# Optimization experiments

Hardware: AMD Instinct MI355X
Metric: run time of the kernel (lower is better)

The kernel has to match this reference:

```python
import jax, jax.numpy as jnp
import numpy as np
from jax import lax

GROUP = 8
EPS = 1e-5

def _bn_relu(x, gamma, beta):
    # BatchNorm3d in train mode: batch stats over (N,D,H,W) per channel, then ReLU
    mean = x.mean(axis=(0, 2, 3, 4), keepdims=True)
    var = x.var(axis=(0, 2, 3, 4), keepdims=True)
    xn = (x - mean) * lax.rsqrt(var + EPS)
    return jax.nn.relu(xn * gamma[None, :, None, None, None] + beta[None, :, None, None, None])

def _group_norm(x, gamma, beta):
    # GroupNorm(cg, cg): one channel per group -> per (n,c) normalization over spatial dims
    mean = x.mean(axis=(2, 3, 4), keepdims=True)
    var = x.var(axis=(2, 3, 4), keepdims=True)
    xn = (x - mean) * lax.rsqrt(var + EPS)
    return xn * gamma[None, :, None, None, None] + beta[None, :, None, None, None]

def setup_inputs() -> dict:
    key = jax.random.key(0)
    ks = jax.random.split(key, 4)
    b, c, d, h, w = 2, 64, 64, 64, 64
    cg = c // GROUP
    return {
        "x": jax.random.normal(ks[0], (b, c, d, h, w), dtype=jnp.float32),
        "conv1_w": jax.random.normal(ks[1], (cg, cg, 1, 1, 1), dtype=jnp.float32) * 0.1,
        "conv1_b": jnp.zeros((cg,), jnp.float32),
        "bn1_g": jnp.ones((cg,), jnp.float32),
        "bn1_b": jnp.zeros((cg,), jnp.float32),
        "conv3_w": jax.random.normal(ks[2], (cg, cg, 3, 3, 3), dtype=jnp.float32) * 0.05,
        "conv3_b": jnp.zeros((cg,), jnp.float32),
        "bn3_g": jnp.ones((cg,), jnp.float32),
        "bn3_b": jnp.zeros((cg,), jnp.float32),
        "gn_g": jnp.ones((cg,), jnp.float32),
        "gn_b": jnp.zeros((cg,), jnp.float32),
    }

def reference(x, conv1_w, conv1_b, bn1_g, bn1_b, conv3_w, conv3_b, bn3_g, bn3_b, gn_g, gn_b):
    b, c, d, h, w = x.shape
    g = GROUP
    cg = c // g
    gx = x.reshape(b * g, cg, d, h, w)

    # directional average pools -> all stacked along axis 2 as length-(d+h+w) profiles
    x_h = gx.mean(axis=(3, 4), keepdims=True)                      # (bg,cg,d,1,1)
    x_w = gx.mean(axis=(2, 4), keepdims=True).transpose(0, 1, 3, 2, 4)  # (bg,cg,h,1,1)
    x_d = gx.mean(axis=(2, 3), keepdims=True).transpose(0, 1, 4, 3, 2)  # (bg,cg,w,1,1)
    cat = jnp.concatenate([x_h, x_w, x_d], axis=2)                 # (bg,cg,d+h+w,1,1)

    # 1x1x1 conv == channel mix, then BN+ReLU
    hwd = jnp.einsum('oi,bisuv->bosuv', conv1_w[:, :, 0, 0, 0], cat) + conv1_b[None, :, None, None, None]
    hwd = _bn_relu(hwd, bn1_g, bn1_b)

    a_h = jax.nn.sigmoid(hwd[:, :, :d]).reshape(b * g, cg, d, 1, 1)
    a_w = jax.nn.sigmoid(hwd[:, :, d:d + h]).reshape(b * g, cg, 1, h, 1)
    a_d = jax.nn.sigmoid(hwd[:, :, d + h:]).reshape(b * g, cg, 1, 1, w)

    x1 = _group_norm(gx * (a_h * a_w * a_d), gn_g, gn_b)           # (bg,cg,d,h,w)

    x2 = lax.conv_general_dilated(gx, conv3_w, (1, 1, 1), 'SAME',
                                  dimension_numbers=('NCDHW', 'OIDHW', 'NCDHW'))
    x2 = _bn_relu(x2 + conv3_b[None, :, None, None, None], bn3_g, bn3_b)

    x11 = jax.nn.softmax(x1.mean(axis=(2, 3, 4)), axis=-1)         # (bg,cg)
    x21 = jax.nn.softmax(x2.mean(axis=(2, 3, 4)), axis=-1)         # (bg,cg)
    x12 = x1.reshape(b * g, cg, d * h * w)
    x22 = x2.reshape(b * g, cg, d * h * w)

    weights = (jnp.einsum('bc,bcn->bn', x11, x22) +
               jnp.einsum('bc,bcn->bn', x21, x12)).reshape(b * g, 1, d, h, w)
    return (gx * jax.nn.sigmoid(weights)).reshape(b, c, d, h, w)
```

## Files before the change

kernel.cpp:

```cpp
#include <hip/hip_runtime.h>
#include <math.h>
#include <stdint.h>

#define VOL 262144
#define EPSF 1e-5f

typedef _Float16 half4_t __attribute__((ext_vector_type(4)));
typedef _Float16 half8 __attribute__((ext_vector_type(8)));
typedef float floatx4 __attribute__((ext_vector_type(4)));

__device__ __forceinline__ float waveReduceSum(float v) {
    #pragma unroll
    for (int off = 32; off > 0; off >>= 1) v += __shfl_down(v, off);
    return v;
}

__device__ __forceinline__ uint32_t pk2(float a, float b) {
    uint32_t r;
    asm("v_cvt_pkrtz_f16_f32 %0, %1, %2" : "=v"(r) : "v"(a), "v"(b));
    return r;
}

__global__ void k_wprep(const float* __restrict__ w3, _Float16* __restrict__ wB) {
    int i = blockIdx.x * 256 + threadIdx.x;
    if (i < 3584) {
        int j = i & 7;
        int lane = (i >> 3) & 63;
        int ks = i >> 9;
        int oc = lane & 15;
        int t = ks * 4 + (lane >> 4);
        float v = 0.f;
        if (oc < 8 && t < 27) v = w3[(oc * 8 + j) * 27 + t];
        wB[i] = (_Float16)v;
    }
}

__global__ void k_pools(const float* __restrict__ x, float* __restrict__ catS) {
    int r = blockIdx.x >> 3, part = blockIdx.x & 7;
    const float* base = x + (size_t)r * VOL + ((size_t)(part * 8) << 12);
    __shared__ float sd[8], sh[64], sw[64];
    int tid = threadIdx.x;
    if (tid < 8) sd[tid] = 0.f;
    if (tid < 64) { sh[tid] = 0.f; sw[tid] = 0.f; }
    __syncthreads();
    int w4 = (tid & 15) * 4;
    int hr = tid >> 4;
    float dacc[8];
    float hacc[4] = {0.f, 0.f, 0.f, 0.f};
    float wacc[4] = {0.f, 0.f, 0.f, 0.f};
    #pragma unroll
    for (int p = 0; p < 8; p++) dacc[p] = 0.f;
    #pragma unroll
    for (int p = 0; p < 8; p++) {
        const float* pd = base + (p << 12);
        #pragma unroll
        for (int j = 0; j < 4; j++) {
            float4 v = *(const float4*)(pd + ((hr + j * 16) << 6) + w4);
            float s = v.x + v.y + v.z + v.w;
            dacc[p] += s; hacc[j] += s;
            wacc[0] += v.x; wacc[1] += v.y; wacc[2] += v.z; wacc[3] += v.w;
        }
    }
    #pragma unroll
    for (int p = 0; p < 8; p++) {
        float s = waveReduceSum(dacc[p]);
        if ((tid & 63) == 0) atomicAdd(&sd[p], s);
    }
    #pragma unroll
    for (int j = 0; j < 4; j++) atomicAdd(&sh[hr + j * 16], hacc[j]);
    #pragma unroll
    for (int k = 0; k < 4; k++) atomicAdd(&sw[w4 + k], wacc[k]);
    __syncthreads();
    float* o = catS + (size_t)r * 192;
    if (tid < 8)                       atomicAdd(&o[part * 8 + tid], sd[tid]);
    else if (tid >= 64 && tid < 128)   atomicAdd(&o[64 + tid - 64], sh[tid - 64]);
    else if (tid >= 128 && tid < 192)  atomicAdd(&o[128 + tid - 128], sw[tid - 128]);
}

__global__ void k_attn_stats(const float* __restrict__ catS, const float* __restrict__ w1,
                             const float* __restrict__ b1, const float* __restrict__ g1,
                             const float* __restrict__ be1, float* __restrict__ attnp) {
    __shared__ float r1[256], r2[256];
    __shared__ float wsm[64];
    int tid = threadIdx.x;
    if (tid < 64) wsm[tid] = w1[tid] * (1.f / 4096.f);
    __syncthreads();
    int o = tid >> 5, j = tid & 31;
    float s1 = 0.f, s2 = 0.f;
    for (int idx = j; idx < 3072; idx += 32) {
        int bgI = idx / 192, s = idx - bgI * 192;
        const float* cp = catS + (size_t)bgI * 1536 + s;
        float h = b1[o];
        #pragma unroll
        for (int i = 0; i < 8; i++) h += wsm[o * 8 + i] * cp[i * 192];
        s1 += h; s2 += h * h;
    }
    r1[tid] = s1; r2[tid] = s2;
    __syncthreads();
    for (int st = 16; st > 0; st >>= 1) {
        if (j < st) { r1[tid] += r1[tid + st]; r2[tid] += r2[tid + st]; }
        __syncthreads();
    }
    if (j == 0) {
        float mean = r1[tid] / 3072.f;
        float var  = r2[tid] / 3072.f - mean * mean;
        float sc = g1[o] * rsqrtf(var + EPSF);
        attnp[o] = sc; attnp[8 + o] = be1[o] - mean * sc;
    }
}

__global__ void k_attn_apply(const float* __restrict__ catS, const float* __restrict__ w1,
                             const float* __restrict__ b1, const float* __restrict__ attnp,
                             float* __restrict__ aout) {
    __shared__ float wsm[64];
    int tid = threadIdx.x;
    if (tid < 64) wsm[tid] = w1[tid] * (1.f / 4096.f);
    __syncthreads();
    int e = blockIdx.x * 256 + tid;
    int bgI = e / 1536;
    int rem = e - bgI * 1536;
    int oo = rem / 192;
    int s = rem - oo * 192;
    const float* cp = catS + (size_t)bgI * 1536 + s;
    float h = b1[oo];
    #pragma unroll
    for (int i = 0; i < 8; i++) h += wsm[oo * 8 + i] * cp[i * 192];
    float v = attnp[oo] * h + attnp[8 + oo];
    v = fmaxf(v, 0.f);
    aout[e] = 1.f / (1.f + __expf(-v));
}

__global__ void k_gnstats(const float* __restrict__ x, const float* __restrict__ a,
                          float* __restrict__ gs) {
    int r = blockIdx.x >> 3, part = blockIdx.x & 7;
    const float* xp = x + (size_t)r * VOL + ((size_t)part << 15);
    __shared__ float A[192];
    __shared__ float wred[8];
    int tid = threadIdx.x;
    if (tid < 192) A[tid] = a[(size_t)r * 192 + tid];
    __syncthreads();
    float s1 = 0.f, s2 = 0.f;
    for (int it = 0; it < 32; it++) {
        int e4 = it * 256 + tid;
        int n = e4 * 4;
        int dl = n >> 12;
        int h = (n >> 6) & 63, w = n & 63;
        float4 v = *(const float4*)(xp + n);
        float adh = A[part * 8 + dl] * A[64 + h];
        float y0 = v.x * adh * A[128 + w];
        float y1 = v.y * adh * A[128 + w + 1];
        float y2 = v.z * adh * A[128 + w + 2];
        float y3 = v.w * adh * A[128 + w + 3];
        s1 += y0 + y1 + y2 + y3;
        s2 += y0 * y0 + y1 * y1 + y2 * y2 + y3 * y3;
    }
    s1 = waveReduceSum(s1); s2 = waveReduceSum(s2);
    int lane = tid & 63, wid = tid >> 6;
    if (lane == 0) { wred[wid] = s1; wred[4 + wid] = s2; }
    __syncthreads();
    if (tid == 0) {
        atomicAdd(&gs[r],       wred[0] + wred[1] + wred[2] + wred[3]);
        atomicAdd(&gs[128 + r], wred[4] + wred[5] + wred[6] + wred[7]);
    }
}

#define SLICE_B (18 * 66 * 16)

__device__ __forceinline__ void stage_slice(const float* __restrict__ xb, int dd,
                                            char* smem, int slot, int h0, int tid) {
    char* sb = smem + slot * SLICE_B;
    bool dok = (dd >= 0) && (dd < 64);
    const float* pd = xb + ((size_t)(dd & 63) << 12);
    for (int u = tid; u < 288; u += 256) {
        int hl = u >> 4;
        int w4 = (u & 15) << 2;
        int gh = h0 - 1 + hl;
        bool ok = dok && (gh >= 0) && (gh < 64);
        float vv[8][4];
        #pragma unroll
        for (int ic = 0; ic < 8; ic++) {
            float4 t = make_float4(0.f, 0.f, 0.f, 0.f);
            if (ok) t = *(const float4*)(pd + ((size_t)ic << 18) + (gh << 6) + w4);
            vv[ic][0] = t.x; vv[ic][1] = t.y; vv[ic][2] = t.z; vv[ic][3] = t.w;
        }
        char* wp = sb + ((hl * 66) + 1 + w4) * 16;
        #pragma unroll
        for (int j = 0; j < 4; j++) {
            uint4 q;
            q.x = pk2(vv[0][j], vv[1][j]);
            q.y = pk2(vv[2][j], vv[3][j]);
            q.z = pk2(vv[4][j], vv[5][j]);
            q.w = pk2(vv[6][j], vv[7][j]);
            *(uint4*)(wp + j * 16) = q;
        }
    }
}

__global__ __launch_bounds__(256) void k_conv(const float* __restrict__ x,
                                              const _Float16* __restrict__ wB,
                                              const float* __restrict__ b3,
                                              _Float16* __restrict__ x2h,
                                              float* __restrict__ stats) {
    __shared__ __align__(16) char smem[3 * SLICE_B + 512];
    float* wred = (float*)(smem + 3 * SLICE_B);
    int blk = blockIdx.x;
    int bg = blk >> 5;
    int rem = blk & 31;
    int ht = rem >> 3;
    int dc = rem & 7;
    int h0 = ht << 4;
    int d0 = dc << 3;
    int tid = threadIdx.x;
    int lane = tid & 63, wid = tid >> 6;
    int lm = lane & 15, lg = lane >> 4;
    const float* xb = x + ((size_t)bg << 21);

    half8 bfr[7];
    #pragma unroll
    for (int ks = 0; ks < 7; ks++)
        bfr[ks] = *(const half8*)(wB + (ks << 9) + (lane << 3));

    float b3v = (lm < 8) ? b3[lm] : 0.f;

    int rel[7], kzv[7];
    #pragma unroll
    for (int ks = 0; ks < 7; ks++) {
        int t = ks * 4 + lg; if (t > 26) t = 26;
        int kz = t / 9, r9 = t - kz * 9;
        int ky = r9 / 3, kx = r9 - ky * 3;
        kzv[ks] = kz;
        rel[ks] = (((ky + wid * 4) * 66) + kx + lm) << 4;
    }

    for (int u = tid; u < 108; u += 256) {
        int s = u / 36, r2 = u - s * 36;
        int hh = r2 >> 1, side = r2 & 1;
        uint4 z; z.x = 0; z.y = 0; z.z = 0; z.w = 0;
        *(uint4*)(smem + s * SLICE_B + ((hh * 66) + side * 65) * 16) = z;
    }

    size_t eb = (((size_t)(bg * 8 + lm)) << 18) + ((size_t)(h0 + wid * 4) << 6) + (lg << 2);
    bool ocok = lm < 8;
    float ps = 0.f, pq = 0.f;

    stage_slice(xb, d0 - 1, smem, (d0 + 2) % 3, h0, tid);
    stage_slice(xb, d0,     smem, d0 % 3,       h0, tid);
    __syncthreads();

    for (int i = 0; i < 8; i++) {
        int d = d0 + i;
        stage_slice(xb, d + 1, smem, (d + 1) % 3, h0, tid);
        __syncthreads();
        int u0 = ((d + 2) % 3) * SLICE_B;
        int u1 = (d % 3) * SLICE_B;
        int u2 = ((d + 1) % 3) * SLICE_B;
        int ab[7];
        #pragma unroll
        for (int ks = 0; ks < 7; ks++)
            ab[ks] = (kzv[ks] == 0 ? u0 : (kzv[ks] == 1 ? u1 : u2)) + rel[ks];
        #pragma unroll
        for (int ri = 0; ri < 4; ri++) {
            #pragma unroll
            for (int wt = 0; wt < 4; wt++) {
                floatx4 acc = {b3v, b3v, b3v, b3v};
                #pragma unroll
                for (int ks = 0; ks < 7; ks++) {
                    half8 af = *(const half8*)(smem + ab[ks] + ((ri * 66 + wt * 16) << 4));
                    acc = __builtin_amdgcn_mfma_f32_16x16x32_f16(af, bfr[ks], acc, 0, 0, 0);
                }
                uint32_t q0 = pk2(acc[0], acc[1]);
                uint32_t q1 = pk2(acc[2], acc[3]);
                if (ocok) {
                    uint2 st; st.x = q0; st.y = q1;
                    *(uint2*)(x2h + eb + ((size_t)d << 12) + (ri << 6) + (wt << 4)) = st;
                }
                ps += acc[0] + acc[1] + acc[2] + acc[3];
                pq += acc[0] * acc[0] + acc[1] * acc[1] + acc[2] * acc[2] + acc[3] * acc[3];
            }
        }
        __syncthreads();
    }

    ps += __shfl_xor(ps, 16); ps += __shfl_xor(ps, 32);
    pq += __shfl_xor(pq, 16); pq += __shfl_xor(pq, 32);
    if (lane < 16) { wred[wid * 32 + lm] = ps; wred[wid * 32 + 16 + lm] = pq; }
    __syncthreads();
    if (tid < 8) {
        float t1 = wred[tid] + wred[32 + tid] + wred[64 + tid] + wred[96 + tid];
        float t2 = wred[16 + tid] + wred[48 + tid] + wred[80 + tid] + wred[112 + tid];
        atomicAdd(&stats[tid], t1);
        atomicAdd(&stats[8 + tid], t2);
    }
}

__global__ void k_finalize(const float* __restrict__ stats, const float* __restrict__ g3,
                           const float* __restrict__ be3, const float* __restrict__ gnb,
                           float* __restrict__ bnp, float* __restrict__ x11) {
    int tid = threadIdx.x;
    if (tid < 8) {
        float N = 16.f * (float)VOL;
        float mean = stats[tid] / N;
        float var  = stats[8 + tid] / N - mean * mean;
        float sc = g3[tid] * rsqrtf(var + EPSF);
        bnp[tid] = sc; bnp[8 + tid] = be3[tid] - mean * sc;
    }
    if (tid == 0) {
        float m = -1e30f;
        for (int c = 0; c < 8; c++) m = fmaxf(m, gnb[c]);
        float e[8], sum = 0.f;
        for (int c = 0; c < 8; c++) { e[c] = __expf(gnb[c] - m); sum += e[c]; }
        for (int c = 0; c < 8; c++) x11[c] = e[c] / sum;
    }
}

__global__ void k_relumean(const _Float16* __restrict__ x2h, const float* __restrict__ bnp,
                           float* __restrict__ mrelu) {
    int blk = blockIdx.x;
    int r = blk >> 3, part = blk & 7;
    int cc = r & 7;
    float sc = bnp[cc], sh = bnp[8 + cc];
    const half4_t* p = (const half4_t*)(x2h + (size_t)r * VOL + (size_t)part * 32768);
    int tid = threadIdx.x;
    float s = 0.f;
    for (int it = 0; it < 32; it++) {
        half4_t v = p[it * 256 + tid];
        s += fmaxf(sc * (float)v.x + sh, 0.f) + fmaxf(sc * (float)v.y + sh, 0.f)
           + fmaxf(sc * (float)v.z + sh, 0.f) + fmaxf(sc * (float)v.w + sh, 0.f);
    }
    s = waveReduceSum(s);
    __shared__ float wred[4];
    int lane = tid & 63, wid = tid >> 6;
    if (lane == 0) wred[wid] = s;
    __syncthreads();
    if (tid == 0) atomicAdd(&mrelu[r], wred[0] + wred[1] + wred[2] + wred[3]);
}

__global__ void k_soft21(const float* __restrict__ mrelu, float* __restrict__ x21) {
    int bg = threadIdx.x;
    if (bg < 16) {
        float v[8], m = -1e30f;
        for (int c = 0; c < 8; c++) { v[c] = mrelu[bg * 8 + c] / (float)VOL; m = fmaxf(m, v[c]); }
        float sum = 0.f;
        for (int c = 0; c < 8; c++) { v[c] = __expf(v[c] - m); sum += v[c]; }
        for (int c = 0; c < 8; c++) x21[bg * 8 + c] = v[c] / sum;
    }
}

__global__ void k_final(const float* __restrict__ x, const _Float16* __restrict__ x2h,
                        const float* __restrict__ a, const float* __restrict__ bnp,
                        const float* __restrict__ x11g, const float* __restrict__ x21g,
                        const float* __restrict__ gs, const float* __restrict__ gng,
                        const float* __restrict__ gnb, float* __restrict__ out) {
    int bg = blockIdx.x >> 8;
    int seg = blockIdx.x & 255;
    int tid = threadIdx.x;
    __shared__ float sa[1536];
    __shared__ float sc_[8], sh_[8], sx11[8], sx21[8], sgsc[8], sgsh[8];
    const float* ap = a + (size_t)bg * 1536;
    for (int i = tid; i < 1536; i += 256) sa[i] = ap[i];
    if (tid < 8) {
        int r = bg * 8 + tid;
        sc_[tid] = bnp[tid]; sh_[tid] = bnp[8 + tid];
        sx11[tid] = x11g[tid]; sx21[tid] = x21g[r];
        float mean = gs[r] / (float)VOL;
        float var  = gs[128 + r] / (float)VOL - mean * mean;
        float gr = rsqrtf(var + EPSF) * gng[tid];
        sgsc[tid] = gr; sgsh[tid] = gnb[tid] - mean * gr;
    }
    __syncthreads();
    int n = (seg * 256 + tid) * 4;
    int d = n >> 12, h = (n >> 6) & 63, w = n & 63;
    size_t base = ((size_t)bg << 21) + n;
    float4 xr[8];
    float w0 = 0.f, w1 = 0.f, w2 = 0.f, w3 = 0.f;
    #pragma unroll
    for (int c = 0; c < 8; c++) {
        size_t idx = base + ((size_t)c << 18);
        float4 xv = *(const float4*)(x + idx);
        half4_t v2 = *(const half4_t*)(x2h + idx);
        xr[c] = xv;
        float adh = sa[c * 192 + d] * sa[c * 192 + 64 + h] * sgsc[c];
        float x22_0 = fmaxf(sc_[c] * (float)v2.x + sh_[c], 0.f);
        float x22_1 = fmaxf(sc_[c] * (float)v2.y + sh_[c], 0.f);
        float x22_2 = fmaxf(sc_[c] * (float)v2.z + sh_[c], 0.f);
        float x22_3 = fmaxf(sc_[c] * (float)v2.w + sh_[c], 0.f);
        float x12_0 = xv.x * (adh * sa[c * 192 + 128 + w])     + sgsh[c];
        float x12_1 = xv.y * (adh * sa[c * 192 + 128 + w + 1]) + sgsh[c];
        float x12_2 = xv.z * (adh * sa[c * 192 + 128 + w + 2]) + sgsh[c];
        float x12_3 = xv.w * (adh * sa[c * 192 + 128 + w + 3]) + sgsh[c];
        w0 += sx11[c] * x22_0 + sx21[c] * x12_0;
        w1 += sx11[c] * x22_1 + sx21[c] * x12_1;
        w2 += sx11[c] * x22_2 + sx21[c] * x12_2;
        w3 += sx11[c] * x22_3 + sx21[c] * x12_3;
    }
    float s0 = 1.f / (1.f + __expf(-w0));
    float s1 = 1.f / (1.f + __expf(-w1));
    float s2 = 1.f / (1.f + __expf(-w2));
    float s3 = 1.f / (1.f + __expf(-w3));
    #pragma unroll
    for (int c = 0; c < 8; c++) {
        float4 o;
        o.x = xr[c].x * s0; o.y = xr[c].y * s1; o.z = xr[c].z * s2; o.w = xr[c].w * s3;
        *(float4*)(out + base + ((size_t)c << 18)) = o;
    }
}

extern "C" void kernel_launch(void* const* d_in, const int* in_sizes, int n_in,
                              void* d_out, int out_size, void* d_ws, size_t ws_size,
                              hipStream_t stream) {
    const float* x   = (const float*)d_in[0];
    const float* w1  = (const float*)d_in[1];
    const float* b1  = (const float*)d_in[2];
    const float* g1  = (const float*)d_in[3];
    const float* be1 = (const float*)d_in[4];
    const float* w3  = (const float*)d_in[5];
    const float* b3  = (const float*)d_in[6];
    const float* g3  = (const float*)d_in[7];
    const float* be3 = (const float*)d_in[8];
    const float* gng = (const float*)d_in[9];
    const float* gnb = (const float*)d_in[10];
    float* out = (float*)d_out;

    float* wsf       = (float*)d_ws;
    _Float16* x2h    = (_Float16*)d_ws;
    float* catS   = wsf + 16777216;
    float* stats  = catS + 24576;
    float* gs     = stats + 16;
    float* mrelu  = gs + 256;
    float* a      = mrelu + 128;
    float* bnp    = a + 24576;
    float* x11    = bnp + 16;
    float* x21    = x11 + 8;
    float* attnp  = x21 + 128;
    _Float16* wB  = (_Float16*)(attnp + 16);

    hipMemsetAsync(catS, 0, (24576 + 16 + 256 + 128) * sizeof(float), stream);

    k_wprep     <<<14, 256, 0, stream>>>(w3, wB);
    k_pools     <<<1024, 256, 0, stream>>>(x, catS);
    k_attn_stats<<<1, 256, 0, stream>>>(catS, w1, b1, g1, be1, attnp);
    k_attn_apply<<<96, 256, 0, stream>>>(catS, w1, b1, attnp, a);
    k_gnstats   <<<1024, 256, 0, stream>>>(x, a, gs);
    k_conv      <<<512, 256, 0, stream>>>(x, wB, b3, x2h, stats);
    k_finalize  <<<1, 64, 0, stream>>>(stats, g3, be3, gnb, bnp, x11);
    k_relumean  <<<1024, 256, 0, stream>>>(x2h, bnp, mrelu);
    k_soft21    <<<1, 64, 0, stream>>>(mrelu, x21);
    k_final     <<<4096, 256, 0, stream>>>(x, x2h, a, bnp, x11, x21, gs, gng, gnb, out);
}
```

Before: 453.6 us.

## Fuse GroupNorm statistics into conv staging and shuffle-reduce pool partials

Removes the separate k_gnstats kernel, which re-read all of x. The conv kernel now accumulates per-channel GroupNorm sums and squared sums while staging x slices, using the attention vectors loaded into shared memory. The pools kernel doubles its grid with 4 depth slices per block and pre-reduces h and w partials with wave shuffles before the shared atomics. This saves one full pass over x in exchange for more register pressure and shared memory in the MFMA conv kernel.

```diff
diff --git a/kernel.cpp b/kernel.cpp
--- a/kernel.cpp
+++ b/kernel.cpp
@@ -36,22 +36,21 @@
 }
 
 __global__ void k_pools(const float* __restrict__ x, float* __restrict__ catS) {
-    int r = blockIdx.x >> 3, part = blockIdx.x & 7;
-    const float* base = x + (size_t)r * VOL + ((size_t)(part * 8) << 12);
-    __shared__ float sd[8], sh[64], sw[64];
-    int tid = threadIdx.x;
-    if (tid < 8) sd[tid] = 0.f;
+    int r = blockIdx.x >> 4, p4 = blockIdx.x & 15;
+    const float* base = x + (size_t)r * VOL + ((size_t)(p4 * 4) << 12);
+    __shared__ float sd[4], sh[64], sw[64];
+    int tid = threadIdx.x;
+    if (tid < 4) sd[tid] = 0.f;
     if (tid < 64) { sh[tid] = 0.f; sw[tid] = 0.f; }
     __syncthreads();
     int w4 = (tid & 15) * 4;
     int hr = tid >> 4;
-    float dacc[8];
+    int lane = tid & 63;
+    float dacc[4] = {0.f, 0.f, 0.f, 0.f};
     float hacc[4] = {0.f, 0.f, 0.f, 0.f};
     float wacc[4] = {0.f, 0.f, 0.f, 0.f};
     #pragma unroll
-    for (int p = 0; p < 8; p++) dacc[p] = 0.f;
-    #pragma unroll
-    for (int p = 0; p < 8; p++) {
+    for (int p = 0; p < 4; p++) {
         const float* pd = base + (p << 12);
         #pragma unroll
         for (int j = 0; j < 4; j++) {
@@ -62,17 +61,26 @@
         }
     }
     #pragma unroll
-    for (int p = 0; p < 8; p++) {
+    for (int p = 0; p < 4; p++) {
         float s = waveReduceSum(dacc[p]);
-        if ((tid & 63) == 0) atomicAdd(&sd[p], s);
-    }
-    #pragma unroll
-    for (int j = 0; j < 4; j++) atomicAdd(&sh[hr + j * 16], hacc[j]);
-    #pragma unroll
-    for (int k = 0; k < 4; k++) atomicAdd(&sw[w4 + k], wacc[k]);
+        if (lane == 0) atomicAdd(&sd[p], s);
+    }
+    #pragma unroll
+    for (int j = 0; j < 4; j++) {
+        float hv = hacc[j];
+        hv += __shfl_xor(hv, 1); hv += __shfl_xor(hv, 2);
+        hv += __shfl_xor(hv, 4); hv += __shfl_xor(hv, 8);
+        if ((lane & 15) == 0) atomicAdd(&sh[hr + j * 16], hv);
+    }
+    #pragma unroll
+    for (int k = 0; k < 4; k++) {
+        float wv = wacc[k];
+        wv += __shfl_xor(wv, 16); wv += __shfl_xor(wv, 32);
+        if (lane < 16) atomicAdd(&sw[w4 + k], wv);
+    }
     __syncthreads();
     float* o = catS + (size_t)r * 192;
-    if (tid < 8)                       atomicAdd(&o[part * 8 + tid], sd[tid]);
+    if (tid < 4)                       atomicAdd(&o[p4 * 4 + tid], sd[tid]);
     else if (tid >= 64 && tid < 128)   atomicAdd(&o[64 + tid - 64], sh[tid - 64]);
     else if (tid >= 128 && tid < 192)  atomicAdd(&o[128 + tid - 128], sw[tid - 128]);
 }
@@ -130,58 +138,41 @@
     aout[e] = 1.f / (1.f + __expf(-v));
 }
 
-__global__ void k_gnstats(const float* __restrict__ x, const float* __restrict__ a,
-                          float* __restrict__ gs) {
-    int r = blockIdx.x >> 3, part = blockIdx.x & 7;
-    const float* xp = x + (size_t)r * VOL + ((size_t)part << 15);
-    __shared__ float A[192];
-    __shared__ float wred[8];
-    int tid = threadIdx.x;
-    if (tid < 192) A[tid] = a[(size_t)r * 192 + tid];
-    __syncthreads();
-    float s1 = 0.f, s2 = 0.f;
-    for (int it = 0; it < 32; it++) {
-        int e4 = it * 256 + tid;
-        int n = e4 * 4;
-        int dl = n >> 12;
-        int h = (n >> 6) & 63, w = n & 63;
-        float4 v = *(const float4*)(xp + n);
-        float adh = A[part * 8 + dl] * A[64 + h];
-        float y0 = v.x * adh * A[128 + w];
-        float y1 = v.y * adh * A[128 + w + 1];
-        float y2 = v.z * adh * A[128 + w + 2];
-        float y3 = v.w * adh * A[128 + w + 3];
-        s1 += y0 + y1 + y2 + y3;
-        s2 += y0 * y0 + y1 * y1 + y2 * y2 + y3 * y3;
-    }
-    s1 = waveReduceSum(s1); s2 = waveReduceSum(s2);
-    int lane = tid & 63, wid = tid >> 6;
-    if (lane == 0) { wred[wid] = s1; wred[4 + wid] = s2; }
-    __syncthreads();
-    if (tid == 0) {
-        atomicAdd(&gs[r],       wred[0] + wred[1] + wred[2] + wred[3]);
-        atomicAdd(&gs[128 + r], wred[4] + wred[5] + wred[6] + wred[7]);
-    }
-}
-
 #define SLICE_B (18 * 66 * 16)
 
 __device__ __forceinline__ void stage_slice(const float* __restrict__ xb, int dd,
-                                            char* smem, int slot, int h0, int tid) {
+                                            char* smem, int slot, int h0, int tid,
+                                            const float* __restrict__ sA, int d0,
+                                            float* g1, float* g2) {
     char* sb = smem + slot * SLICE_B;
     bool dok = (dd >= 0) && (dd < 64);
+    bool core = (dd >= d0) && (dd < d0 + 8);
     const float* pd = xb + ((size_t)(dd & 63) << 12);
     for (int u = tid; u < 288; u += 256) {
         int hl = u >> 4;
         int w4 = (u & 15) << 2;
         int gh = h0 - 1 + hl;
         bool ok = dok && (gh >= 0) && (gh < 64);
+        bool acc = core && (hl >= 1) && (hl <= 16);
         float vv[8][4];
         #pragma unroll
         for (int ic = 0; ic < 8; ic++) {
             float4 t = make_float4(0.f, 0.f, 0.f, 0.f);
             if (ok) t = *(const float4*)(pd + ((size_t)ic << 18) + (gh << 6) + w4);
             vv[ic][0] = t.x; vv[ic][1] = t.y; vv[ic][2] = t.z; vv[ic][3] = t.w;
+        }
+        if (acc) {
+            #pragma unroll
+            for (int ic = 0; ic < 8; ic++) {
+                const float* Ap = sA + ic * 192;
+                float ad = Ap[dd] * Ap[64 + gh];
+                float y0 = vv[ic][0] * ad * Ap[128 + w4];
+                float y1 = vv[ic][1] * ad * Ap[128 + w4 + 1];
+                float y2 = vv[ic][2] * ad * Ap[128 + w4 + 2];
+                float y3 = vv[ic][3] * ad * Ap[128 + w4 + 3];
+                g1[ic] += y0 + y1 + y2 + y3;
+                g2[ic] += y0 * y0 + y1 * y1 + y2 * y2 + y3 * y3;
+            }
         }
         char* wp = sb + ((hl * 66) + 1 + w4) * 16;
         #pragma unroll
@@ -199,10 +190,14 @@
 __global__ __launch_bounds__(256) void k_conv(const float* __restrict__ x,
                                               const _Float16* __restrict__ wB,
                                               const float* __restrict__ b3,
+                                              const float* __restrict__ a,
                                               _Float16* __restrict__ x2h,
-                                              float* __restrict__ stats) {
-    __shared__ __align__(16) char smem[3 * SLICE_B + 512];
+                                              float* __restrict__ stats,
+                                              float* __restrict__ gs) {
+    __shared__ __align__(16) char smem[3 * SLICE_B + 768 + 6144];
     float* wred = (float*)(smem + 3 * SLICE_B);
+    float* wgn  = wred + 128;
+    float* sA   = (float*)(smem + 3 * SLICE_B + 768);
     int blk = blockIdx.x;
     int bg = blk >> 5;
     int rem = blk & 31;
@@ -238,18 +233,22 @@
         uint4 z; z.x = 0; z.y = 0; z.z = 0; z.w = 0;
         *(uint4*)(smem + s * SLICE_B + ((hh * 66) + side * 65) * 16) = z;
     }
+    for (int i = tid; i < 1536; i += 256) sA[i] = a[(size_t)bg * 1536 + i];
+    __syncthreads();
 
     size_t eb = (((size_t)(bg * 8 + lm)) << 18) + ((size_t)(h0 + wid * 4) << 6) + (lg << 2);
     bool ocok = lm < 8;
     float ps = 0.f, pq = 0.f;
-
-    stage_slice(xb, d0 - 1, smem, (d0 + 2) % 3, h0, tid);
-    stage_slice(xb, d0,     smem, d0 % 3,       h0, tid);
+    float g1[8] = {0.f, 0.f, 0.f, 0.f, 0.f, 0.f, 0.f, 0.f};
+    float g2[8] = {0.f, 0.f, 0.f, 0.f, 0.f, 0.f, 0.f, 0.f};
+
+    stage_slice(xb, d0 - 1, smem, (d0 + 2) % 3, h0, tid, sA, d0, g1, g2);
+    stage_slice(xb, d0,     smem, d0 % 3,       h0, tid, sA, d0, g1, g2);
     __syncthreads();
 
     for (int i = 0; i < 8; i++) {
         int d = d0 + i;
-        stage_slice(xb, d + 1, smem, (d + 1) % 3, h0, tid);
+        stage_slice(xb, d + 1, smem, (d + 1) % 3, h0, tid, sA, d0, g1, g2);
         __syncthreads();
         int u0 = ((d + 2) % 3) * SLICE_B;
         int u1 = (d % 3) * SLICE_B;
@@ -284,12 +283,22 @@
     ps += __shfl_xor(ps, 16); ps += __shfl_xor(ps, 32);
     pq += __shfl_xor(pq, 16); pq += __shfl_xor(pq, 32);
     if (lane < 16) { wred[wid * 32 + lm] = ps; wred[wid * 32 + 16 + lm] = pq; }
+    #pragma unroll
+    for (int ic = 0; ic < 8; ic++) {
+        float r1v = waveReduceSum(g1[ic]);
+        float r2v = waveReduceSum(g2[ic]);
+        if (lane == 0) { wgn[wid * 16 + ic] = r1v; wgn[wid * 16 + 8 + ic] = r2v; }
+    }
     __syncthreads();
     if (tid < 8) {
         float t1 = wred[tid] + wred[32 + tid] + wred[64 + tid] + wred[96 + tid];
         float t2 = wred[16 + tid] + wred[48 + tid] + wred[80 + tid] + wred[112 + tid];
         atomicAdd(&stats[tid], t1);
         atomicAdd(&stats[8 + tid], t2);
+        float q1 = wgn[tid] + wgn[16 + tid] + wgn[32 + tid] + wgn[48 + tid];
+        float q2 = wgn[8 + tid] + wgn[24 + tid] + wgn[40 + tid] + wgn[56 + tid];
+        atomicAdd(&gs[bg * 8 + tid], q1);
+        atomicAdd(&gs[128 + bg * 8 + tid], q2);
     }
 }
 
@@ -437,11 +446,10 @@
     hipMemsetAsync(catS, 0, (24576 + 16 + 256 + 128) * sizeof(float), stream);
 
     k_wprep     <<<14, 256, 0, stream>>>(w3, wB);
-    k_pools     <<<1024, 256, 0, stream>>>(x, catS);
+    k_pools     <<<2048, 256, 0, stream>>>(x, catS);
     k_attn_stats<<<1, 256, 0, stream>>>(catS, w1, b1, g1, be1, attnp);
     k_attn_apply<<<96, 256, 0, stream>>>(catS, w1, b1, attnp, a);
-    k_gnstats   <<<1024, 256, 0, stream>>>(x, a, gs);
-    k_conv      <<<512, 256, 0, stream>>>(x, wB, b3, x2h, stats);
+    k_conv      <<<512, 256, 0, stream>>>(x, wB, b3, a, x2h, stats, gs);
     k_finalize  <<<1, 64, 0, stream>>>(stats, g3, be3, gnb, bnp, x11);
     k_relumean  <<<1024, 256, 0, stream>>>(x2h, bnp, mrelu);
     k_soft21    <<<1, 64, 0, stream>>>(mrelu, x21);
```

Measured after the change: 430.9 us. 5.0% less time.
